# Performance work log

Hardware: AMD Instinct MI355X
Metric: run time of the kernel (lower is better)

The kernel has to match this reference:

```python
import jax, jax.numpy as jnp
import numpy as np

KH = KW = 3
STRIDE = 1
PAD = 1
DIL = 1


def _conv2d(x, w, b):
    out = jax.lax.conv_general_dilated(
        x, w, (STRIDE, STRIDE), [(PAD, PAD), (PAD, PAD)],
        rhs_dilation=(DIL, DIL), dimension_numbers=('NCHW', 'OIHW', 'NCHW'))
    return out + b[None, :, None, None]


def _bilinear_sample(x, ys, xs):
    # x: [B,C,H,W]; ys, xs: [B,K,Ho,Wo] float sampling coords (zero padding outside)
    B, C, H, W = x.shape
    y0 = jnp.floor(ys)
    x0 = jnp.floor(xs)
    wy1 = ys - y0
    wx1 = xs - x0
    wy0 = 1.0 - wy1
    wx0 = 1.0 - wx1
    x_flat = x.reshape(B, C, H * W)

    def gather(yc, xc):
        valid = (yc >= 0) & (yc <= H - 1) & (xc >= 0) & (xc <= W - 1)
        yi = jnp.clip(yc, 0, H - 1).astype(jnp.int32)
        xi = jnp.clip(xc, 0, W - 1).astype(jnp.int32)
        idx = yi * W + xi  # [B,K,Ho,Wo]
        g = jax.vmap(lambda xb, ib: xb[:, ib.reshape(-1)])(x_flat, idx)
        g = g.reshape(B, C, *idx.shape[1:])  # [B,C,K,Ho,Wo]
        return g * valid[:, None].astype(x.dtype)

    return (gather(y0, x0) * (wy0 * wx0)[:, None]
            + gather(y0, x0 + 1) * (wy0 * wx1)[:, None]
            + gather(y0 + 1, x0) * (wy1 * wx0)[:, None]
            + gather(y0 + 1, x0 + 1) * (wy1 * wx1)[:, None])


def setup_inputs() -> dict:
    key = jax.random.key(0)
    ks = jax.random.split(key, 6)
    B, C, H, W = 8, 256, 64, 64
    Cout = 256
    K = KH * KW
    x = jax.random.normal(ks[0], (B, C, H, W), jnp.float32)
    # small random offset/mask heads (module inits them to zero; random keeps the
    # irregular-gather path exercised with modest, realistic offsets)
    w_offset = jax.random.normal(ks[1], (2 * K, C, KH, KW), jnp.float32) * 0.01
    b_offset = jax.random.normal(ks[2], (2 * K,), jnp.float32) * 0.1
    w_mask = jax.random.normal(ks[3], (K, C, KH, KW), jnp.float32) * 0.01
    b_mask = jnp.zeros((K,), jnp.float32)
    stdv = 1.0 / np.sqrt(C * KH * KW)
    weight = jax.random.uniform(ks[4], (Cout, C, KH, KW), jnp.float32, -stdv, stdv)
    bias = jnp.zeros((Cout,), jnp.float32)
    return {"x": x, "w_offset": w_offset, "b_offset": b_offset,
            "w_mask": w_mask, "b_mask": b_mask, "weight": weight, "bias": bias}


def reference(x, w_offset, b_offset, w_mask, b_mask, weight, bias):
    B, C, H, W = x.shape
    K = KH * KW
    offset = _conv2d(x, w_offset, b_offset)          # [B, 2K, Ho, Wo]
    mask = jax.nn.sigmoid(_conv2d(x, w_mask, b_mask))  # [B, K, Ho, Wo]
    Ho, Wo = offset.shape[2], offset.shape[3]
    off = offset.reshape(B, K, 2, Ho, Wo)
    dy, dx = off[:, :, 0], off[:, :, 1]              # (dy, dx) pairs per kernel tap
    ky = jnp.arange(KH, dtype=x.dtype) * DIL - PAD
    kx = jnp.arange(KW, dtype=x.dtype) * DIL - PAD
    kyf = jnp.repeat(ky, KW)   # [K]
    kxf = jnp.tile(kx, KH)     # [K]
    ys = jnp.arange(Ho, dtype=x.dtype)[None, None, :, None] * STRIDE + kyf[None, :, None, None] + dy
    xs = jnp.arange(Wo, dtype=x.dtype)[None, None, None, :] * STRIDE + kxf[None, :, None, None] + dx
    sampled = _bilinear_sample(x, ys, xs) * mask[:, None]  # [B,C,K,Ho,Wo]
    out = jnp.einsum('bckhw,ock->bohw', sampled, weight.reshape(weight.shape[0], C, K))
    return out + bias[None, :, None, None]
```

## Files before the change

kernel.cpp:

```cpp
#include <hip/hip_runtime.h>
#include <math.h>


typedef __bf16 bf16x8 __attribute__((ext_vector_type(8)));
typedef float  f32x4  __attribute__((ext_vector_type(4)));
typedef float  f32x2  __attribute__((ext_vector_type(2)));
typedef int    i32x4  __attribute__((ext_vector_type(4)));
typedef unsigned short u16x8 __attribute__((ext_vector_type(8)));
typedef unsigned short u16x4 __attribute__((ext_vector_type(4)));

__device__ __forceinline__ unsigned short f2b(float f) {
  return __builtin_bit_cast(unsigned short, (__bf16)f);
}
__device__ __forceinline__ float blo(unsigned u) {
  return __builtin_bit_cast(float, u << 16);
}
__device__ __forceinline__ float bhi(unsigned u) {
  return __builtin_bit_cast(float, u & 0xffff0000u);
}
__device__ __forceinline__ void lds_barrier() {
  asm volatile("s_waitcnt lgkmcnt(0)" ::: "memory");
  __builtin_amdgcn_s_barrier();
}

__global__ __launch_bounds__(256) void transpose_nhwc(const float* __restrict__ x,
                                                      unsigned short* __restrict__ xt) {
  __shared__ float tile[64][65];
  const int bid = blockIdx.x;
  const int b = bid & 7, rem = bid >> 3;
  const int cc = rem & 3, hw0 = (rem >> 2) << 6;
  const int t = threadIdx.x;
  const int a = t & 63, g = t >> 6;
#pragma unroll
  for (int r = 0; r < 16; ++r) {
    int crow = (r << 2) + g;
    tile[crow][a] = x[(((b << 8) + (cc << 6) + crow) << 12) + hw0 + a];
  }
  __syncthreads();
  const int a0 = (t & 15) << 2, gg = t >> 4;
#pragma unroll
  for (int r = 0; r < 4; ++r) {
    int hwr = (r << 4) + gg;
    u16x4 v;
#pragma unroll
    for (int j = 0; j < 4; ++j) v[j] = f2b(tile[a0 + j][hwr]);
    *(u16x4*)&xt[((b << 12) + hw0 + hwr) * 256 + (cc << 6) + a0] = v;
  }
}

__global__ __launch_bounds__(256) void pack_w(const float* __restrict__ w,
                                              __bf16* __restrict__ wp) {
  int idx = blockIdx.x * 256 + threadIdx.x;
  if (idx >= 256 * 256 * 9) return;
  int o = idx / 2304, rem = idx - o * 2304;
  int c = rem / 9, k = rem - c * 9;
  wp[(((k << 5) + (c >> 3)) * 256 + o) * 8 + (c & 7)] = (__bf16)w[idx];
}

__global__ __launch_bounds__(256) void pack_wom(const float* __restrict__ wo,
                                                const float* __restrict__ wm,
                                                __bf16* __restrict__ wp) {
  int idx = blockIdx.x * 256 + threadIdx.x;
  if (idx >= 32 * 256 * 9) return;
  int r = idx / 2304, rem = idx - r * 2304;
  int c = rem / 9, k = rem - c * 9;
  float v = 0.f;
  if (r < 18) v = wo[((r << 8) + c) * 9 + k];
  else if (r < 27) v = wm[(((r - 18) << 8) + c) * 9 + k];
  wp[(((k << 5) + (c >> 3)) * 32 + r) * 8 + (c & 7)] = (__bf16)v;
}

__global__ __launch_bounds__(256) void offset_conv(
    const unsigned short* __restrict__ xt, const __bf16* __restrict__ wp,
    const float* __restrict__ b_off, const float* __restrict__ b_msk,
    float* __restrict__ dyp, float* __restrict__ dxp, float* __restrict__ mkp) {
  const int bi = blockIdx.x & 7, h = blockIdx.x >> 3;
  const int t = threadIdx.x, lane = t & 63, nw = t >> 6;
  const int l16 = lane & 15, lh = lane >> 4;
  __shared__ __align__(16) unsigned short S[2][64 * 64];
  f32x4 acc[2] = {};
  const int sp = t >> 2, sc0 = (t & 3) << 4;
  const int g0 = (t & 3) << 1;
  const int w0 = (sp << 6) + (((g0 ^ (sp & 7)) & 7) << 3);
  const int w1 = (sp << 6) + ((((g0 + 1) ^ (sp & 7)) & 7) << 3);
  const long xb = (long)bi << 20;

  auto LOAD = [&](int it, u16x8* r) {
    const int k = it >> 2, cc = it & 3;
    const int hh = h + k / 3 - 1;
    const int ww = sp + k % 3 - 1;
    const bool valid = (hh >= 0) & (hh < 64) & (ww >= 0) & (ww < 64);
    if (valid) {
      const unsigned short* src = xt + xb + (((hh << 6) + ww) << 8) + (cc << 6) + sc0;
      r[0] = *(const u16x8*)src;
      r[1] = *(const u16x8*)(src + 8);
    } else {
      r[0] = u16x8{}; r[1] = u16x8{};
    }
  };

  auto STEP = [&](int it, const u16x8* r, int buf) {
    unsigned short* Sb = S[buf];
    *(u16x8*)&Sb[w0] = r[0];
    *(u16x8*)&Sb[w1] = r[1];
    lds_barrier();
    const int k = it >> 2, cc = it & 3;
#pragma unroll
    for (int kk = 0; kk < 2; ++kk) {
      const int prow = (nw << 4) + l16;
      const int gi = (kk << 2) | lh;
      bf16x8 bfrag = *(const bf16x8*)&Sb[(prow << 6) + (((gi ^ (prow & 7)) & 7) << 3)];
#pragma unroll
      for (int mf = 0; mf < 2; ++mf) {
        const __bf16* ap = wp + ((((k << 5) + (cc << 3) + (kk << 2) + lh) << 5) + (mf << 4) + l16) * 8;
        bf16x8 af = *(const bf16x8*)ap;
        acc[mf] = __builtin_amdgcn_mfma_f32_16x16x32_bf16(af, bfrag, acc[mf], 0, 0, 0);
      }
    }
  };

  u16x8 rA[2], rB[2];
  LOAD(0, rA);
  for (int it = 0; it < 36; it += 2) {
    LOAD(it + 1, rB);
    STEP(it, rA, 0);
    if (it + 2 < 36) LOAD(it + 2, rA);
    STEP(it + 1, rB, 1);
  }

  const int p = (nw << 4) + l16;
  const int hw = (h << 6) + p;
#pragma unroll
  for (int mf = 0; mf < 2; ++mf) {
#pragma unroll
    for (int r = 0; r < 4; ++r) {
      int row = (mf << 4) + (lh << 2) + r;
      float v = acc[mf][r];
      if (row < 18) {
        v += b_off[row];
        float* dst = (row & 1) ? dxp : dyp;
        dst[(((bi * 9) + (row >> 1)) << 12) + hw] = v;
      } else if (row < 27) {
        int km = row - 18;
        v += b_msk[km];
        mkp[(((bi * 9) + km) << 12) + hw] = 1.f / (1.f + expf(-v));
      }
    }
  }
}

__global__ __launch_bounds__(512, 4) void deform_gemm(
    const unsigned short* __restrict__ xt, const __bf16* __restrict__ wp,
    const float* __restrict__ dyp, const float* __restrict__ dxp,
    const float* __restrict__ mkp, const float* __restrict__ bias,
    float* __restrict__ out) {
  const int bi = blockIdx.x & 7, h = blockIdx.x >> 3;
  const int t = threadIdx.x, lane = t & 63, wv = t >> 6;
  const int l16 = lane & 15, lh = lane >> 4;
  __shared__ __align__(16) unsigned short S[2][64 * 64];
  __shared__ __align__(16) float samp[9][64][8];

  for (int i = t; i < 576; i += 512) {
    int k = i >> 6, p = i & 63;
    int idx = (((bi * 9) + k) << 12) + (h << 6) + p;
    float dy = dyp[idx], dx = dxp[idx], mk = mkp[idx];
    float ys = (float)(h + k / 3 - 1) + dy;
    float xs = (float)(p + k % 3 - 1) + dx;
    float y0f = floorf(ys), x0f = floorf(xs);
    int iy0 = (int)y0f, ix0 = (int)x0f;
    float wy1 = ys - y0f, wx1 = xs - x0f;
    float wy0 = 1.f - wy1, wx0 = 1.f - wx1;
    float w00 = wy0 * wx0 * mk, w01 = wy0 * wx1 * mk;
    float w10 = wy1 * wx0 * mk, w11 = wy1 * wx1 * mk;
    if (iy0 < 0 || iy0 > 63) { w00 = 0.f; w01 = 0.f; }
    if (iy0 < -1 || iy0 > 62) { w10 = 0.f; w11 = 0.f; }
    if (ix0 < 0 || ix0 > 63) { w00 = 0.f; w10 = 0.f; }
    if (ix0 < -1 || ix0 > 62) { w01 = 0.f; w11 = 0.f; }
    const int cy0 = min(max(iy0, 0), 63), cy1 = min(max(iy0 + 1, 0), 63);
    const int cx0 = min(max(ix0, 0), 63), cx1 = min(max(ix0 + 1, 0), 63);
    samp[k][p][0] = w00; samp[k][p][1] = w01;
    samp[k][p][2] = w10; samp[k][p][3] = w11;
    samp[k][p][4] = __builtin_bit_cast(float, (((cy0 << 6) + cx0) << 8));
    samp[k][p][5] = __builtin_bit_cast(float, (((cy0 << 6) + cx1) << 8));
    samp[k][p][6] = __builtin_bit_cast(float, (((cy1 << 6) + cx0) << 8));
    samp[k][p][7] = __builtin_bit_cast(float, (((cy1 << 6) + cx1) << 8));
  }
  __syncthreads();

  f32x4 acc[2][4] = {};
  const int sp = t >> 3;
  const int sc0 = (t & 7) << 3;
  const int wofs = (sp << 6) + ((((t & 7) ^ (sp & 7)) & 7) << 3);
  const unsigned short* xtb = xt + ((long)bi << 20);

  auto GATHER = [&](int it, u16x8* r, f32x4& w4) {
    const int k = it >> 2, cc = it & 3;
    w4 = *(const f32x4*)&samp[k][sp][0];
    i32x4 o4 = __builtin_bit_cast(i32x4, *(const f32x4*)&samp[k][sp][4]);
    const int c0 = (cc << 6) + sc0;
    r[0] = *(const u16x8*)(xtb + o4.x + c0);
    r[1] = *(const u16x8*)(xtb + o4.y + c0);
    r[2] = *(const u16x8*)(xtb + o4.z + c0);
    r[3] = *(const u16x8*)(xtb + o4.w + c0);
  };

  auto STEP = [&](int it, const u16x8* r, const f32x4& w4, int buf) {
    u16x8 sv;
    const unsigned* u0 = (const unsigned*)&r[0];
    const unsigned* u1 = (const unsigned*)&r[1];
    const unsigned* u2 = (const unsigned*)&r[2];
    const unsigned* u3 = (const unsigned*)&r[3];
#pragma unroll
    for (int j = 0; j < 4; ++j) {
      f32x2 a{blo(u0[j]), bhi(u0[j])};
      f32x2 b{blo(u1[j]), bhi(u1[j])};
      f32x2 c{blo(u2[j]), bhi(u2[j])};
      f32x2 d{blo(u3[j]), bhi(u3[j])};
      f32x2 s = a * w4.x;
      s += b * w4.y;
      s += c * w4.z;
      s += d * w4.w;
      sv[2 * j]     = f2b(s.x);
      sv[2 * j + 1] = f2b(s.y);
    }
    *(u16x8*)&S[buf][wofs] = sv;
    lds_barrier();
    const int k = it >> 2, cc = it & 3;
#pragma unroll
    for (int kk = 0; kk < 2; ++kk) {
      bf16x8 bfr[4];
#pragma unroll
      for (int nf = 0; nf < 4; ++nf) {
        const int prow = (nf << 4) + l16;
        const int gi = (kk << 2) | lh;
        bfr[nf] = *(const bf16x8*)&S[buf][(prow << 6) + (((gi ^ (prow & 7)) & 7) << 3)];
      }
#pragma unroll
      for (int mf = 0; mf < 2; ++mf) {
        const int orow = (wv << 5) + (mf << 4) + l16;
        const __bf16* ap = wp + ((((k << 5) + (cc << 3) + (kk << 2) + lh) << 8) + orow) * 8;
        bf16x8 af = *(const bf16x8*)ap;
#pragma unroll
        for (int nf = 0; nf < 4; ++nf)
          acc[mf][nf] = __builtin_amdgcn_mfma_f32_16x16x32_bf16(af, bfr[nf], acc[mf][nf], 0, 0, 0);
      }
    }
  };

  u16x8 rA[4], rB[4];
  f32x4 wA, wB;
  GATHER(0, rA, wA);
  for (int it = 0; it < 36; it += 2) {
    GATHER(it + 1, rB, wB);
    STEP(it, rA, wA, 0);
    if (it + 2 < 36) GATHER(it + 2, rA, wA);
    STEP(it + 1, rB, wB, 1);
  }

#pragma unroll
  for (int mf = 0; mf < 2; ++mf) {
    const int o = (wv << 5) + (mf << 4) + (lh << 2);
    f32x4 bv = *(const f32x4*)(bias + o);
#pragma unroll
    for (int nf = 0; nf < 4; ++nf) {
      const int p = (nf << 4) + l16;
      const int hw = (h << 6) + p;
#pragma unroll
      for (int r = 0; r < 4; ++r)
        out[(((bi << 8) + o + r) << 12) + hw] = acc[mf][nf][r] + bv[r];
    }
  }
}

extern "C" void kernel_launch(void* const* d_in, const int* in_sizes, int n_in,
                              void* d_out, int out_size, void* d_ws, size_t ws_size,
                              hipStream_t stream) {
  (void)in_sizes; (void)n_in; (void)out_size; (void)ws_size;
  const float* x        = (const float*)d_in[0];
  const float* w_offset = (const float*)d_in[1];
  const float* b_offset = (const float*)d_in[2];
  const float* w_mask   = (const float*)d_in[3];
  const float* b_mask   = (const float*)d_in[4];
  const float* weight   = (const float*)d_in[5];
  const float* bias     = (const float*)d_in[6];
  float* out = (float*)d_out;

  char* ws = (char*)d_ws;
  unsigned short* xt = (unsigned short*)(ws);
  __bf16* Wpack  = (__bf16*)(ws + 16777216);
  __bf16* Womp   = (__bf16*)(ws + 17956864);
  float*  dyp    = (float*)(ws + 18104320);
  float*  dxp    = (float*)(ws + 19283968);
  float*  mkp    = (float*)(ws + 20463616);

  transpose_nhwc<<<2048, 256, 0, stream>>>(x, xt);
  pack_w<<<2304, 256, 0, stream>>>(weight, Wpack);
  pack_wom<<<288, 256, 0, stream>>>(w_offset, w_mask, Womp);
  offset_conv<<<512, 256, 0, stream>>>(xt, Womp, b_offset, b_mask, dyp, dxp, mkp);
  deform_gemm<<<512, 512, 0, stream>>>(xt, Wpack, dyp, dxp, mkp, bias, out);
}
```

Before: 106.3 us.

## Double K-step per barrier in deform GEMM and merge weight pack kernels

The deformable GEMM now gathers and interpolates two K-chunks per period into a doubled LDS buffer, so it hits a barrier half as often and keeps more gathers in flight (8 vector loads per buffer). To fit the extra registers, the occupancy hint drops from 4 to 2 blocks per CU. The two weight-packing kernels are merged into a single launch to save one kernel launch. Possible costs are higher register pressure, more LDS per block and less latency hiding from fewer resident waves.

```diff
diff --git a/kernel.cpp b/kernel.cpp
--- a/kernel.cpp
+++ b/kernel.cpp
@@ -48,26 +48,26 @@
   }
 }
 
-__global__ __launch_bounds__(256) void pack_w(const float* __restrict__ w,
-                                              __bf16* __restrict__ wp) {
-  int idx = blockIdx.x * 256 + threadIdx.x;
-  if (idx >= 256 * 256 * 9) return;
-  int o = idx / 2304, rem = idx - o * 2304;
-  int c = rem / 9, k = rem - c * 9;
-  wp[(((k << 5) + (c >> 3)) * 256 + o) * 8 + (c & 7)] = (__bf16)w[idx];
-}
-
-__global__ __launch_bounds__(256) void pack_wom(const float* __restrict__ wo,
+__global__ __launch_bounds__(256) void pack_all(const float* __restrict__ w,
+                                                const float* __restrict__ wo,
                                                 const float* __restrict__ wm,
-                                                __bf16* __restrict__ wp) {
-  int idx = blockIdx.x * 256 + threadIdx.x;
-  if (idx >= 32 * 256 * 9) return;
-  int r = idx / 2304, rem = idx - r * 2304;
-  int c = rem / 9, k = rem - c * 9;
-  float v = 0.f;
-  if (r < 18) v = wo[((r << 8) + c) * 9 + k];
-  else if (r < 27) v = wm[(((r - 18) << 8) + c) * 9 + k];
-  wp[(((k << 5) + (c >> 3)) * 32 + r) * 8 + (c & 7)] = (__bf16)v;
+                                                __bf16* __restrict__ wp,
+                                                __bf16* __restrict__ womp) {
+  if (blockIdx.x < 2304) {
+    int idx = blockIdx.x * 256 + threadIdx.x;
+    int o = idx / 2304, rem = idx - o * 2304;
+    int c = rem / 9, k = rem - c * 9;
+    wp[(((k << 5) + (c >> 3)) * 256 + o) * 8 + (c & 7)] = (__bf16)w[idx];
+  } else {
+    int idx = (blockIdx.x - 2304) * 256 + threadIdx.x;
+    if (idx >= 32 * 256 * 9) return;
+    int r = idx / 2304, rem = idx - r * 2304;
+    int c = rem / 9, k = rem - c * 9;
+    float v = 0.f;
+    if (r < 18) v = wo[((r << 8) + c) * 9 + k];
+    else if (r < 27) v = wm[(((r - 18) << 8) + c) * 9 + k];
+    womp[(((k << 5) + (c >> 3)) * 32 + r) * 8 + (c & 7)] = (__bf16)v;
+  }
 }
 
 __global__ __launch_bounds__(256) void offset_conv(
@@ -149,7 +149,7 @@
   }
 }
 
-__global__ __launch_bounds__(512, 4) void deform_gemm(
+__global__ __launch_bounds__(512, 2) void deform_gemm(
     const unsigned short* __restrict__ xt, const __bf16* __restrict__ wp,
     const float* __restrict__ dyp, const float* __restrict__ dxp,
     const float* __restrict__ mkp, const float* __restrict__ bias,
@@ -157,7 +157,7 @@
   const int bi = blockIdx.x & 7, h = blockIdx.x >> 3;
   const int t = threadIdx.x, lane = t & 63, wv = t >> 6;
   const int l16 = lane & 15, lh = lane >> 4;
-  __shared__ __align__(16) unsigned short S[2][64 * 64];
+  __shared__ __align__(16) unsigned short S[2][2][64 * 64];
   __shared__ __align__(16) float samp[9][64][8];
 
   for (int i = t; i < 576; i += 512) {
@@ -204,7 +204,7 @@
     r[3] = *(const u16x8*)(xtb + o4.w + c0);
   };
 
-  auto STEP = [&](int it, const u16x8* r, const f32x4& w4, int buf) {
+  auto INTERP_WRITE = [&](const u16x8* r, const f32x4& w4, unsigned short* dst) {
     u16x8 sv;
     const unsigned* u0 = (const unsigned*)&r[0];
     const unsigned* u1 = (const unsigned*)&r[1];
@@ -223,38 +223,52 @@
       sv[2 * j]     = f2b(s.x);
       sv[2 * j + 1] = f2b(s.y);
     }
-    *(u16x8*)&S[buf][wofs] = sv;
+    *(u16x8*)dst = sv;
+  };
+
+  auto PERIOD = [&](int it, const u16x8* r, const f32x4& w4a, const f32x4& w4b, int buf) {
+    INTERP_WRITE(r,     w4a, &S[buf][0][wofs]);
+    INTERP_WRITE(r + 4, w4b, &S[buf][1][wofs]);
     lds_barrier();
-    const int k = it >> 2, cc = it & 3;
-#pragma unroll
-    for (int kk = 0; kk < 2; ++kk) {
-      bf16x8 bfr[4];
-#pragma unroll
-      for (int nf = 0; nf < 4; ++nf) {
-        const int prow = (nf << 4) + l16;
-        const int gi = (kk << 2) | lh;
-        bfr[nf] = *(const bf16x8*)&S[buf][(prow << 6) + (((gi ^ (prow & 7)) & 7) << 3)];
+#pragma unroll
+    for (int half = 0; half < 2; ++half) {
+      const int itc = it + half;
+      const int k = itc >> 2, cc = itc & 3;
+#pragma unroll
+      for (int kk = 0; kk < 2; ++kk) {
+        bf16x8 bfr[4];
+#pragma unroll
+        for (int nf = 0; nf < 4; ++nf) {
+          const int prow = (nf << 4) + l16;
+          const int gi = (kk << 2) | lh;
+          bfr[nf] = *(const bf16x8*)&S[buf][half][(prow << 6) + (((gi ^ (prow & 7)) & 7) << 3)];
+        }
+#pragma unroll
+        for (int mf = 0; mf < 2; ++mf) {
+          const int orow = (wv << 5) + (mf << 4) + l16;
+          const __bf16* ap = wp + ((((k << 5) + (cc << 3) + (kk << 2) + lh) << 8) + orow) * 8;
+          bf16x8 af = *(const bf16x8*)ap;
+#pragma unroll
+          for (int nf = 0; nf < 4; ++nf)
+            acc[mf][nf] = __builtin_amdgcn_mfma_f32_16x16x32_bf16(af, bfr[nf], acc[mf][nf], 0, 0, 0);
+        }
       }
-#pragma unroll
-      for (int mf = 0; mf < 2; ++mf) {
-        const int orow = (wv << 5) + (mf << 4) + l16;
-        const __bf16* ap = wp + ((((k << 5) + (cc << 3) + (kk << 2) + lh) << 8) + orow) * 8;
-        bf16x8 af = *(const bf16x8*)ap;
-#pragma unroll
-        for (int nf = 0; nf < 4; ++nf)
-          acc[mf][nf] = __builtin_amdgcn_mfma_f32_16x16x32_bf16(af, bfr[nf], acc[mf][nf], 0, 0, 0);
-      }
-    }
-  };
-
-  u16x8 rA[4], rB[4];
-  f32x4 wA, wB;
-  GATHER(0, rA, wA);
-  for (int it = 0; it < 36; it += 2) {
-    GATHER(it + 1, rB, wB);
-    STEP(it, rA, wA, 0);
-    if (it + 2 < 36) GATHER(it + 2, rA, wA);
-    STEP(it + 1, rB, wB, 1);
+    }
+  };
+
+  u16x8 rA[8], rB[8];
+  f32x4 wA0, wA1, wB0, wB1;
+  GATHER(0, rA, wA0);
+  GATHER(1, rA + 4, wA1);
+  for (int it = 0; it < 36; it += 4) {
+    GATHER(it + 2, rB, wB0);
+    GATHER(it + 3, rB + 4, wB1);
+    PERIOD(it, rA, wA0, wA1, 0);
+    if (it + 4 < 36) {
+      GATHER(it + 4, rA, wA0);
+      GATHER(it + 5, rA + 4, wA1);
+    }
+    PERIOD(it + 2, rB, wB0, wB1, 1);
   }
 
 #pragma unroll
@@ -294,8 +308,7 @@
   float*  mkp    = (float*)(ws + 20463616);
 
   transpose_nhwc<<<2048, 256, 0, stream>>>(x, xt);
-  pack_w<<<2304, 256, 0, stream>>>(weight, Wpack);
-  pack_wom<<<288, 256, 0, stream>>>(w_offset, w_mask, Womp);
+  pack_all<<<2592, 256, 0, stream>>>(weight, w_offset, w_mask, Wpack, Womp);
   offset_conv<<<512, 256, 0, stream>>>(xt, Womp, b_offset, b_mask, dyp, dxp, mkp);
   deform_gemm<<<512, 512, 0, stream>>>(xt, Wpack, dyp, dxp, mkp, bias, out);
 }
```

Measured after the change: 126.3 us. 1.19x slower.
